# Kernel optimization log

Measured on AMD Instinct MI355X. Metric: run time of the kernel, lower is better.

## Reference

```python
import jax, jax.numpy as jnp
import numpy as np

BASE_DIM = 256
FIBER_DIM = 64
BATCH = 4096
PATH_LEN = 512


def setup_inputs() -> dict:
    key = jax.random.key(0)
    k1, k2, k3 = jax.random.split(key, 3)
    fiber_state = jax.random.normal(k1, (BATCH, FIBER_DIM), dtype=jnp.float32)
    base_path = jax.random.uniform(k2, (BATCH, PATH_LEN), dtype=jnp.float32)
    # torch init is identity expanded over base_dim; add small noise so the
    # learned parameter is non-trivial while repeated products stay bounded.
    connection = (jnp.eye(FIBER_DIM, dtype=jnp.float32)[None, :, :]
                  + 0.01 * jax.random.normal(k3, (BASE_DIM, FIBER_DIM, FIBER_DIM), dtype=jnp.float32))
    return {"fiber_state": fiber_state, "base_path": base_path, "connection": connection}


def reference(fiber_state, base_path, connection):
    # fiber_state: [B, f]; base_path: [B, L]; connection: [base_dim, f, f]
    base_dim = connection.shape[0]
    xs = base_path[:, :-1].T  # [L-1, B], one path step per scan iteration

    def step(t, bp):
        # per-step index derived from path values, normalized by batch max (clamped at 1)
        mx = jnp.maximum(jnp.max(bp), 1.0)
        idx = jnp.clip((bp * base_dim / mx).astype(jnp.int32), 0, base_dim - 1)  # [B]
        mats = connection[idx]  # [B, f, f] gather
        t = jnp.einsum('bi,bij->bj', t, mats)  # row-vector times matrix (torch bmm of [B,1,f]x[B,f,f])
        return t, None

    transported, _ = jax.lax.scan(step, fiber_state, xs)
    return transported
```

## Files before the change

### kernel.cpp

```cpp
#include <hip/hip_runtime.h>
#include <stdint.h>

#define BATCH 4096
#define PLEN  512
#define NSTEP 511
#define FD    64


__global__ void k_init_colmax(unsigned int* cm) {
    int t = threadIdx.x;
    if (t < PLEN) cm[t] = 0x3f800000u;
}

__global__ void k_colmax(const float* __restrict__ bp, unsigned int* __restrict__ cm) {
    __shared__ float red[256];
    int tx = threadIdx.x & 63;
    int ty = threadIdx.x >> 6;
    int t  = blockIdx.x * 64 + tx;
    int b0 = blockIdx.y * 256 + ty * 64;
    const float* p = bp + (size_t)b0 * PLEN + t;
    float m = 0.0f;
    #pragma unroll 4
    for (int r = 0; r < 64; ++r) {
        m = fmaxf(m, p[(size_t)r * PLEN]);
    }
    red[threadIdx.x] = m;
    __syncthreads();
    if (ty == 0) {
        m = fmaxf(fmaxf(red[tx], red[64 + tx]), fmaxf(red[128 + tx], red[192 + tx]));
        atomicMax((int*)&cm[t], __float_as_int(m));
    }
}

__device__ __forceinline__ unsigned short f2h(float x) {
    _Float16 h = (_Float16)x;
    return __builtin_bit_cast(unsigned short, h);
}

__global__ void k_idx_pack(const float* __restrict__ bp, const unsigned int* __restrict__ cm,
                           uint8_t* __restrict__ idx, const float* __restrict__ conn,
                           uint4* __restrict__ ph) {
    int bid = blockIdx.x;
    if (bid < (BATCH * PLEN) / 256) {
        int gid = bid * 256 + threadIdx.x;
        int t = gid & (PLEN - 1);
        uint8_t k = 0;
        if (t < NSTEP) {
            float mx = __uint_as_float(cm[t]);
            float v  = bp[gid];
            float q  = (v * 256.0f) / mx;
            int ik = (int)q;
            ik = ik < 0 ? 0 : (ik > 255 ? 255 : ik);
            k = (uint8_t)ik;
        }
        idx[gid] = k;
    } else {
        int gid = (bid - (BATCH * PLEN) / 256) * 256 + threadIdx.x;
        int j = gid & 63;
        int m = (gid >> 6) & 7;
        int k = gid >> 9;
        const float* M = conn + ((size_t)k << 12);
        unsigned int w[4];
        #pragma unroll
        for (int d = 0; d < 4; ++d) {
            int i0 = 8 * m + 2 * d, i1 = i0 + 1;
            float x0 = M[i0 * 64 + j] - (i0 == j ? 1.0f : 0.0f);
            float x1 = M[i1 * 64 + j] - (i1 == j ? 1.0f : 0.0f);
            w[d] = (unsigned)f2h(x0) | ((unsigned)f2h(x1) << 16);
        }
        ph[gid] = make_uint4(w[0], w[1], w[2], w[3]);
    }
}

#define MIX_LL(P, BW, MW) \
    asm("v_fma_mix_f32 %0, %1, %2, %0 op_sel_hi:[1,1,0]" : "+v"(P) : "v"(BW), "v"(MW))
#define MIX_HH(P, BW, MW) \
    asm("v_fma_mix_f32 %0, %1, %2, %0 op_sel:[1,1,0] op_sel_hi:[1,1,0]" : "+v"(P) : "v"(BW), "v"(MW))

__device__ __forceinline__ float step16h(float acc, const uint4 buf[8],
                                         unsigned short* sah, int lane) {
    ((_Float16*)sah)[lane] = (_Float16)acc;
    asm volatile("s_waitcnt lgkmcnt(0)" ::: "memory");
    float p0 = acc, p1 = 0.f, p2 = 0.f, p3 = 0.f;
    const uint4* sv = (const uint4*)sah;
    #pragma unroll
    for (int q = 0; q < 8; ++q) {
        uint4 B = buf[q];
        uint4 W = sv[q];
        MIX_LL(p0, W.x, B.x); MIX_HH(p1, W.x, B.x);
        MIX_LL(p2, W.y, B.y); MIX_HH(p3, W.y, B.y);
        MIX_LL(p0, W.z, B.z); MIX_HH(p1, W.z, B.z);
        MIX_LL(p2, W.w, B.w); MIX_HH(p3, W.w, B.w);
    }
    return (p0 + p1) + (p2 + p3);
}

__global__ void __launch_bounds__(256) k_chain(
    const float* __restrict__ fiber, const uint8_t* __restrict__ idx,
    const uint4* __restrict__ ph, float* __restrict__ out)
{
    __shared__ uint64_t sidx64[4][64];
    __shared__ __align__(16) unsigned short sah[4][64];
    int wid  = threadIdx.x >> 6;
    int lane = threadIdx.x & 63;
    int b = blockIdx.x * 4 + wid;

    sidx64[wid][lane] = ((const uint64_t*)(idx + (size_t)b * PLEN))[lane];
    __syncthreads();
    const uint8_t* si = (const uint8_t*)sidx64[wid];
    unsigned short* sa = &sah[wid][0];

    float acc = fiber[b * FD + lane];

    uint4 bufA[8], bufB[8];

    int k0 = __builtin_amdgcn_readfirstlane((int)si[0]);
    {
        const uint4* M = ph + ((size_t)k0 << 9);
        #pragma unroll
        for (int m = 0; m < 8; ++m) bufA[m] = M[m * 64 + lane];
    }
    int kn = (int)si[1];

    #pragma unroll 1
    for (int i = 0; i < 255; ++i) {
        int kb = __builtin_amdgcn_readfirstlane(kn);
        {
            const uint4* M = ph + ((size_t)kb << 9);
            #pragma unroll
            for (int m = 0; m < 8; ++m) bufB[m] = M[m * 64 + lane];
        }
        int kn2 = (int)si[2 * i + 2];
        acc = step16h(acc, bufA, sa, lane);
        int ka = __builtin_amdgcn_readfirstlane(kn2);
        {
            const uint4* M = ph + ((size_t)ka << 9);
            #pragma unroll
            for (int m = 0; m < 8; ++m) bufA[m] = M[m * 64 + lane];
        }
        kn = (int)si[2 * i + 3];
        acc = step16h(acc, bufB, sa, lane);
    }
    acc = step16h(acc, bufA, sa, lane);

    out[b * FD + lane] = acc;
}

extern "C" void kernel_launch(void* const* d_in, const int* in_sizes, int n_in,
                              void* d_out, int out_size, void* d_ws, size_t ws_size,
                              hipStream_t stream) {
    const float* fiber = (const float*)d_in[0];
    const float* bp    = (const float*)d_in[1];
    const float* conn  = (const float*)d_in[2];
    float* out = (float*)d_out;

    unsigned int* cm = (unsigned int*)d_ws;
    uint8_t* idx = (uint8_t*)d_ws + 2048;
    uint4* ph = (uint4*)((uint8_t*)d_ws + 2048 + (size_t)BATCH * PLEN);

    hipLaunchKernelGGL(k_init_colmax, dim3(1), dim3(512), 0, stream, cm);
    hipLaunchKernelGGL(k_colmax, dim3(8, 16), dim3(256), 0, stream, bp, cm);
    hipLaunchKernelGGL(k_idx_pack, dim3((BATCH * PLEN) / 256 + 512), dim3(256), 0, stream,
                       bp, cm, idx, conn, ph);
    hipLaunchKernelGGL(k_chain, dim3(BATCH / 4), dim3(256), 0, stream, fiber, idx, ph, out);
}
```

Baseline: 527.1 us.

## Split each batch row's matvec across two wavefronts with LDS partial-sum exchange

Each batch element is now handled by two wavefronts. Each computes half of the 64-row reduction using half of the packed matrix, and the two exchange partial sums through shared memory after a block barrier every step. This doubles the number of waves working on the sequential chain and halves the per-wave register buffers. In exchange it adds a __syncthreads and LDS round trip on every one of the 511 serial steps, plus a higher occupancy target in the launch bounds.

```diff
diff --git a/kernel.cpp b/kernel.cpp
--- a/kernel.cpp
+++ b/kernel.cpp
@@ -77,16 +77,16 @@
 #define MIX_HH(P, BW, MW) \
     asm("v_fma_mix_f32 %0, %1, %2, %0 op_sel:[1,1,0] op_sel_hi:[1,1,0]" : "+v"(P) : "v"(BW), "v"(MW))
 
-__device__ __forceinline__ float step16h(float acc, const uint4 buf[8],
-                                         unsigned short* sah, int lane) {
+__device__ __forceinline__ float half_partial(float acc, const uint4 buf[4],
+                                              unsigned short* sah, int lane, int wid) {
     ((_Float16*)sah)[lane] = (_Float16)acc;
     asm volatile("s_waitcnt lgkmcnt(0)" ::: "memory");
-    float p0 = acc, p1 = 0.f, p2 = 0.f, p3 = 0.f;
+    float p0 = 0.f, p1 = 0.f, p2 = 0.f, p3 = 0.f;
     const uint4* sv = (const uint4*)sah;
     #pragma unroll
-    for (int q = 0; q < 8; ++q) {
+    for (int q = 0; q < 4; ++q) {
+        uint4 W = sv[4 * wid + q];
         uint4 B = buf[q];
-        uint4 W = sv[q];
         MIX_LL(p0, W.x, B.x); MIX_HH(p1, W.x, B.x);
         MIX_LL(p2, W.y, B.y); MIX_HH(p3, W.y, B.y);
         MIX_LL(p0, W.z, B.z); MIX_HH(p1, W.z, B.z);
@@ -95,30 +95,38 @@
     return (p0 + p1) + (p2 + p3);
 }
 
-__global__ void __launch_bounds__(256) k_chain(
+__global__ void __launch_bounds__(256, 8) k_chain(
     const float* __restrict__ fiber, const uint8_t* __restrict__ idx,
     const uint4* __restrict__ ph, float* __restrict__ out)
 {
-    __shared__ uint64_t sidx64[4][64];
+    __shared__ uint32_t sidx32[2][128];
     __shared__ __align__(16) unsigned short sah[4][64];
-    int wid  = threadIdx.x >> 6;
+    __shared__ float pslot[2][2][2][64];
+
+    int wv   = threadIdx.x >> 6;
+    int h    = wv >> 1;
+    int wid  = wv & 1;
     int lane = threadIdx.x & 63;
-    int b = blockIdx.x * 4 + wid;
+    int b    = blockIdx.x * 2 + h;
 
-    sidx64[wid][lane] = ((const uint64_t*)(idx + (size_t)b * PLEN))[lane];
+    sidx32[h][threadIdx.x & 127] =
+        ((const uint32_t*)(idx + (size_t)b * PLEN))[threadIdx.x & 127];
     __syncthreads();
-    const uint8_t* si = (const uint8_t*)sidx64[wid];
-    unsigned short* sa = &sah[wid][0];
+    const uint8_t* si = (const uint8_t*)sidx32[h];
+    unsigned short* sa = &sah[wv][0];
+    float* ps0 = &pslot[h][0][0][0];
+    float* ps1 = &pslot[h][1][0][0];
 
     float acc = fiber[b * FD + lane];
 
-    uint4 bufA[8], bufB[8];
+    uint4 bufA[4], bufB[4];
+    const uint4* phw = ph + (size_t)wid * 4 * 64;
 
     int k0 = __builtin_amdgcn_readfirstlane((int)si[0]);
     {
-        const uint4* M = ph + ((size_t)k0 << 9);
+        const uint4* M = phw + ((size_t)k0 << 9);
         #pragma unroll
-        for (int m = 0; m < 8; ++m) bufA[m] = M[m * 64 + lane];
+        for (int m = 0; m < 4; ++m) bufA[m] = M[m * 64 + lane];
     }
     int kn = (int)si[1];
 
@@ -126,24 +134,42 @@
     for (int i = 0; i < 255; ++i) {
         int kb = __builtin_amdgcn_readfirstlane(kn);
         {
-            const uint4* M = ph + ((size_t)kb << 9);
+            const uint4* M = phw + ((size_t)kb << 9);
             #pragma unroll
-            for (int m = 0; m < 8; ++m) bufB[m] = M[m * 64 + lane];
+            for (int m = 0; m < 4; ++m) bufB[m] = M[m * 64 + lane];
         }
         int kn2 = (int)si[2 * i + 2];
-        acc = step16h(acc, bufA, sa, lane);
+        {
+            float P = half_partial(acc, bufA, sa, lane, wid);
+            ps0[wid * 64 + lane] = P;
+            __syncthreads();
+            float other = ps0[(wid ^ 1) * 64 + lane];
+            acc = acc + (P + other);
+        }
         int ka = __builtin_amdgcn_readfirstlane(kn2);
         {
-            const uint4* M = ph + ((size_t)ka << 9);
+            const uint4* M = phw + ((size_t)ka << 9);
             #pragma unroll
-            for (int m = 0; m < 8; ++m) bufA[m] = M[m * 64 + lane];
+            for (int m = 0; m < 4; ++m) bufA[m] = M[m * 64 + lane];
         }
         kn = (int)si[2 * i + 3];
-        acc = step16h(acc, bufB, sa, lane);
+        {
+            float P = half_partial(acc, bufB, sa, lane, wid);
+            ps1[wid * 64 + lane] = P;
+            __syncthreads();
+            float other = ps1[(wid ^ 1) * 64 + lane];
+            acc = acc + (P + other);
+        }
     }
-    acc = step16h(acc, bufA, sa, lane);
+    {
+        float P = half_partial(acc, bufA, sa, lane, wid);
+        ps0[wid * 64 + lane] = P;
+        __syncthreads();
+        float other = ps0[(wid ^ 1) * 64 + lane];
+        acc = acc + (P + other);
+    }
 
-    out[b * FD + lane] = acc;
+    if (wid == 0) out[b * FD + lane] = acc;
 }
 
 extern "C" void kernel_launch(void* const* d_in, const int* in_sizes, int n_in,
@@ -162,5 +188,5 @@
     hipLaunchKernelGGL(k_colmax, dim3(8, 16), dim3(256), 0, stream, bp, cm);
     hipLaunchKernelGGL(k_idx_pack, dim3((BATCH * PLEN) / 256 + 512), dim3(256), 0, stream,
                        bp, cm, idx, conn, ph);
-    hipLaunchKernelGGL(k_chain, dim3(BATCH / 4), dim3(256), 0, stream, fiber, idx, ph, out);
+    hipLaunchKernelGGL(k_chain, dim3(BATCH / 2), dim3(256), 0, stream, fiber, idx, ph, out);
 }
```

After: 575.0 us. +9.1%, slower.
